# Kernel optimization log

Hardware: AMD Instinct MI355X
Metric: run time of the kernel (lower is better)

The kernel has to match this reference:

```python
import jax, jax.numpy as jnp
import numpy as np

EPS = 1e-5
NUM_HEAD = 8
HEAD_DIM = 64
SCALE = HEAD_DIM ** -0.5


def setup_inputs() -> dict:
    key = jax.random.key(0)
    ks = jax.random.split(key, 3)
    b, n, dim = 4, 2048, 512
    inner = NUM_HEAD * HEAD_DIM  # 512
    x = jax.random.normal(ks[0], (b, n, dim), dtype=jnp.float32)
    ln_w = jnp.ones((dim,), jnp.float32)
    ln_b = jnp.zeros((dim,), jnp.float32)
    qkv_w = jax.random.normal(ks[1], (3 * inner, dim), jnp.float32) * (dim ** -0.5)
    qkv_b = jnp.zeros((3 * inner,), jnp.float32)
    out_w = jax.random.normal(ks[2], (dim, inner), jnp.float32) * (inner ** -0.5)
    out_b = jnp.zeros((dim,), jnp.float32)
    return {"x": x, "ln_w": ln_w, "ln_b": ln_b, "qkv_w": qkv_w,
            "qkv_b": qkv_b, "out_w": out_w, "out_b": out_b}


def reference(x, ln_w, ln_b, qkv_w, qkv_b, out_w, out_b):
    b, n, dim = x.shape
    # Pre-norm LayerNorm
    mu = jnp.mean(x, axis=-1, keepdims=True)
    var = jnp.mean(jnp.square(x - mu), axis=-1, keepdims=True)
    xn = (x - mu) * jax.lax.rsqrt(var + EPS) * ln_w + ln_b
    # QKV projection (torch Linear: y = x @ W.T + b)
    qkv = xn @ qkv_w.T + qkv_b  # [b, n, 3*inner]
    q, k, v = jnp.split(qkv, 3, axis=-1)
    def heads(t):  # [b, n, inner] -> [b, h, n, d]
        return t.reshape(b, n, NUM_HEAD, HEAD_DIM).transpose(0, 2, 1, 3)
    q, k, v = heads(q), heads(k), heads(v)
    # Naive full attention (materializes [b, h, n, n])
    dots = jnp.einsum('bhqd,bhkd->bhqk', q, k) * SCALE
    attn = jax.nn.softmax(dots, axis=-1)
    o = jnp.einsum('bhqk,bhkd->bhqd', attn, v)
    o = o.transpose(0, 2, 1, 3).reshape(b, n, NUM_HEAD * HEAD_DIM)
    return o @ out_w.T + out_b
```

## Files before the change

kernel.cpp:

```cpp
#include <hip/hip_runtime.h>

typedef __attribute__((ext_vector_type(8))) short bf16x8;
typedef __attribute__((ext_vector_type(4))) float floatx4;

#define B_    4
#define N_    2048
#define DIM_  512
#define NH_   8
#define HD_   64
#define SCALE_ 0.125f
#define SL2E_ (0.125f * 1.44269504f)

__device__ __forceinline__ unsigned short f32_to_bf16(float f) {
    unsigned int u = __float_as_uint(f);
    u += 0x7FFFu + ((u >> 16) & 1u);
    return (unsigned short)(u >> 16);
}

__device__ __forceinline__ float bf16_to_f32(unsigned short u) {
    return __uint_as_float(((unsigned int)u) << 16);
}

__device__ __forceinline__ floatx4 mfma16(bf16x8 a, bf16x8 b, floatx4 c) {
    return __builtin_amdgcn_mfma_f32_16x16x32_bf16(a, b, c, 0, 0, 0);
}

__device__ __forceinline__ floatx4 fzero4() {
    floatx4 z = {0.f, 0.f, 0.f, 0.f};
    return z;
}

__device__ __forceinline__ void async16(const unsigned short* g, unsigned short* l) {
    __builtin_amdgcn_global_load_lds((const __attribute__((address_space(1))) void*)g,
                                     (__attribute__((address_space(3))) void*)l,
                                     16, 0, 0);
}

__global__ __launch_bounds__(256) void ln_kernel(const float* __restrict__ x,
                                                 const float* __restrict__ w,
                                                 const float* __restrict__ b,
                                                 unsigned short* __restrict__ xn) {
    int row = blockIdx.x;
    int tid = threadIdx.x;
    int lane = tid & 63, wid = tid >> 6;
    const float2 v = ((const float2*)(x + (size_t)row * DIM_))[tid];
    float s = v.x + v.y;
    float sq = v.x * v.x + v.y * v.y;
#pragma unroll
    for (int off = 1; off < 64; off <<= 1) {
        s  += __shfl_xor(s, off, 64);
        sq += __shfl_xor(sq, off, 64);
    }
    __shared__ float red[2][4];
    if (lane == 0) { red[0][wid] = s; red[1][wid] = sq; }
    __syncthreads();
    s  = red[0][0] + red[0][1] + red[0][2] + red[0][3];
    sq = red[1][0] + red[1][1] + red[1][2] + red[1][3];
    float mu   = s * (1.f / DIM_);
    float var  = sq * (1.f / DIM_) - mu * mu;
    float rstd = rsqrtf(var + 1e-5f);
    float2 wv = ((const float2*)w)[tid];
    float2 bv = ((const float2*)b)[tid];
    float y0 = (v.x - mu) * rstd * wv.x + bv.x;
    float y1 = (v.y - mu) * rstd * wv.y + bv.y;
    unsigned int pack = (unsigned int)f32_to_bf16(y0) |
                        ((unsigned int)f32_to_bf16(y1) << 16);
    ((unsigned int*)xn)[(size_t)row * (DIM_ / 2) + tid] = pack;
}

__global__ __launch_bounds__(256) void cvt_kernel(const float* __restrict__ srcA, int na,
                                                  const float* __restrict__ srcB, int nb,
                                                  unsigned short* __restrict__ dstA,
                                                  unsigned short* __restrict__ dstB) {
    int idx = blockIdx.x * 256 + threadIdx.x;
    if (idx < na)            dstA[idx] = f32_to_bf16(srcA[idx]);
    else if (idx < na + nb)  dstB[idx - na] = f32_to_bf16(srcB[idx - na]);
}

#define GEMM_CORE512(A_, B_ptr, am0, bn0)                                           \
    __shared__ unsigned short Alds[2][128][32];                                     \
    __shared__ unsigned short Blds[2][128][32];                                     \
    int tid = threadIdx.x, lane = tid & 63, wid = tid >> 6;                         \
    int l15 = lane & 15, quad = lane >> 4;                                          \
    int wmloc = (wid >> 1) * 32, wnloc = (wid & 1) * 64;                            \
    int sr = lane >> 2;                                                             \
    int sc = (lane & 3) * 8;                                                        \
    int srow0 = 16 * wid;                                                           \
    floatx4 acc[2][4];                                                              \
    _Pragma("unroll")                                                               \
    for (int i = 0; i < 2; i++)                                                     \
        _Pragma("unroll")                                                           \
        for (int j = 0; j < 4; j++) acc[i][j] = fzero4();                           \
    int buf = 0;                                                                    \
    async16(A_ + (size_t)(am0 + srow0 + sr) * DIM_ + sc, &Alds[0][srow0][0]);       \
    async16(B_ptr + (size_t)(bn0 + srow0 + sr) * DIM_ + sc, &Blds[0][srow0][0]);    \
    __syncthreads();                                                                \
    for (int t = 0; t < 16; t++) {                                                  \
        if (t < 15) {                                                               \
            int k0 = (t + 1) * 32;                                                  \
            async16(A_ + (size_t)(am0 + srow0 + sr) * DIM_ + k0 + sc,               \
                    &Alds[buf ^ 1][srow0][0]);                                      \
            async16(B_ptr + (size_t)(bn0 + srow0 + sr) * DIM_ + k0 + sc,            \
                    &Blds[buf ^ 1][srow0][0]);                                      \
        }                                                                           \
        bf16x8 av[2], bv[4];                                                        \
        _Pragma("unroll")                                                           \
        for (int i = 0; i < 2; i++)                                                 \
            av[i] = *(const bf16x8*)(&Alds[buf][wmloc + 16 * i + l15][quad * 8]);   \
        _Pragma("unroll")                                                           \
        for (int j = 0; j < 4; j++)                                                 \
            bv[j] = *(const bf16x8*)(&Blds[buf][wnloc + 16 * j + l15][quad * 8]);   \
        _Pragma("unroll")                                                           \
        for (int i = 0; i < 2; i++)                                                 \
            _Pragma("unroll")                                                       \
            for (int j = 0; j < 4; j++)                                             \
                acc[i][j] = mfma16(av[i], bv[j], acc[i][j]);                        \
        __syncthreads();                                                            \
        buf ^= 1;                                                                   \
    }

__global__ __launch_bounds__(512, 4) void qkv_gemm(const unsigned short* __restrict__ A,
                                                   const unsigned short* __restrict__ Bw,
                                                   const float* __restrict__ bias,
                                                   unsigned short* __restrict__ Qh,
                                                   unsigned short* __restrict__ Kh,
                                                   unsigned short* __restrict__ Vt) {
    int am0 = blockIdx.x * 128, bn0 = blockIdx.y * 128;
    GEMM_CORE512(A, Bw, am0, bn0)

    if (bn0 >= 1024) {
        unsigned short* sc_ = &Alds[0][0][0] + wid * (16 * 40);
        int m0 = am0 + wmloc;
        int bidx = m0 >> 11;
        int t0 = m0 & 2047;
#pragma unroll
        for (int j = 0; j < 4; j++) {
            float bias_n = bias[bn0 + wnloc + 16 * j + l15];
#pragma unroll
            for (int i = 0; i < 2; i++)
#pragma unroll
                for (int r = 0; r < 4; r++)
                    sc_[l15 * 40 + 16 * i + quad * 4 + r] =
                        f32_to_bf16(acc[i][j][r] + bias_n);
            int nr = lane >> 2;
            int rem = (bn0 - 1024) + wnloc + 16 * j + nr;
            int head = rem >> 6, d = rem & 63;
            bf16x8 vv = *(const bf16x8*)(sc_ + nr * 40 + (lane & 3) * 8);
            *(bf16x8*)(Vt + ((size_t)(bidx * NH_ + head) * HD_ + d) * N_ +
                       t0 + (lane & 3) * 8) = vv;
        }
    } else {
#pragma unroll
        for (int i = 0; i < 2; i++) {
#pragma unroll
            for (int j = 0; j < 4; j++) {
                int n = bn0 + wnloc + 16 * j + l15;
                float bias_n = bias[n];
                int which = n >> 9;
                int rem = n & 511;
                int head = rem >> 6;
                int d = rem & 63;
#pragma unroll
                for (int r = 0; r < 4; r++) {
                    int m = am0 + wmloc + 16 * i + quad * 4 + r;
                    int b = m >> 11;
                    int t = m & 2047;
                    float val = acc[i][j][r] + bias_n;
                    if (which == 0) {
                        Qh[((size_t)(b * NH_ + head) * N_ + t) * HD_ + d] =
                            f32_to_bf16(val * SL2E_);
                    } else {
                        Kh[((size_t)(b * NH_ + head) * N_ + t) * HD_ + d] =
                            f32_to_bf16(val);
                    }
                }
            }
        }
    }
}

__global__ __launch_bounds__(512, 4) void out_gemm(const unsigned short* __restrict__ A,
                                                   const unsigned short* __restrict__ Bw,
                                                   const float* __restrict__ bias,
                                                   float* __restrict__ out) {
    int am0 = blockIdx.x * 128, bn0 = blockIdx.y * 128;
    GEMM_CORE512(A, Bw, am0, bn0)

#pragma unroll
    for (int i = 0; i < 2; i++) {
#pragma unroll
        for (int j = 0; j < 4; j++) {
            int n = bn0 + wnloc + 16 * j + l15;
            float bias_n = bias[n];
#pragma unroll
            for (int r = 0; r < 4; r++) {
                int m = am0 + wmloc + 16 * i + quad * 4 + r;
                out[(size_t)m * DIM_ + n] = acc[i][j][r] + bias_n;
            }
        }
    }
}

__global__ __launch_bounds__(256, 4) void attn_kernel(const unsigned short* __restrict__ Qh,
                                                      const unsigned short* __restrict__ Kh,
                                                      const unsigned short* __restrict__ Vtg,
                                                      unsigned short* __restrict__ Opart,
                                                      float* __restrict__ lpart) {
    int bh = blockIdx.y;
    int b = bh >> 3, head = bh & 7;
    int qt = blockIdx.x;
    int split = blockIdx.z;
    int kv0 = split << 10;
    int tid = threadIdx.x, lane = tid & 63, w = tid >> 6;
    int l15 = lane & 15, quad = lane >> 4;

    const unsigned short* Qp = Qh + (size_t)bh * N_ * HD_;
    const unsigned short* Kg = Kh + (size_t)bh * N_ * HD_;
    const unsigned short* Vg = Vtg + (size_t)bh * HD_ * N_;

    int q0 = qt * 128 + w * 32;

    bf16x8 aQ[2][2];
#pragma unroll
    for (int mh = 0; mh < 2; mh++) {
        const unsigned short* qrow = Qp + (size_t)(q0 + mh * 16 + l15) * HD_ + quad * 8;
        aQ[mh][0] = *(const bf16x8*)(qrow);
        aQ[mh][1] = *(const bf16x8*)(qrow + 32);
    }

    floatx4 of[2][4];
#pragma unroll
    for (int mh = 0; mh < 2; mh++)
#pragma unroll
        for (int t = 0; t < 4; t++) of[mh][t] = fzero4();
    floatx4 lacc[2];
    lacc[0] = fzero4(); lacc[1] = fzero4();

    const short onebf = (short)0x3F80;
    bf16x8 ones = {onebf, onebf, onebf, onebf, onebf, onebf, onebf, onebf};

    __shared__ unsigned short Kt[64][64];
    __shared__ unsigned short Vs[64][64];
    __shared__ unsigned short Pl[4][32][72];

    int srow = lane >> 3;
    int scol = ((lane & 7) ^ srow) * 8;

    int swz0 = (quad ^ (l15 & 7)) * 8;
    int swz1 = ((quad + 4) ^ (l15 & 7)) * 8;

    unsigned short* myP = &Pl[w][0][0];
    for (int kv = kv0; kv < kv0 + 1024; kv += 64) {
#pragma unroll
        for (int i = 0; i < 2; i++) {
            int r0 = 16 * w + 8 * i;
            async16(Kg + (size_t)(kv + r0 + srow) * HD_ + scol, &Kt[r0][0]);
            async16(Vg + (size_t)(r0 + srow) * N_ + kv + scol, &Vs[r0][0]);
        }
        __syncthreads();
        bf16x8 kf[8];
#pragma unroll
        for (int h = 0; h < 4; h++) {
            kf[2 * h]     = *(const bf16x8*)(&Kt[16 * h + l15][swz0]);
            kf[2 * h + 1] = *(const bf16x8*)(&Kt[16 * h + l15][swz1]);
        }
#pragma unroll
        for (int mh = 0; mh < 2; mh++) {
            floatx4 c[4];
#pragma unroll
            for (int h = 0; h < 4; h++) {
                floatx4 cc = fzero4();
                cc = mfma16(aQ[mh][0], kf[2 * h], cc);
                cc = mfma16(aQ[mh][1], kf[2 * h + 1], cc);
                c[h] = cc;
            }
            unsigned short* pw = myP + (mh * 16 + quad * 4) * 72 + l15;
#pragma unroll
            for (int h = 0; h < 4; h++)
#pragma unroll
                for (int r = 0; r < 4; r++)
                    pw[r * 72 + h * 16] = f32_to_bf16(exp2f(c[h][r]));
        }
        bf16x8 vf[8];
#pragma unroll
        for (int t = 0; t < 4; t++) {
            vf[2 * t]     = *(const bf16x8*)(&Vs[16 * t + l15][swz0]);
            vf[2 * t + 1] = *(const bf16x8*)(&Vs[16 * t + l15][swz1]);
        }
#pragma unroll
        for (int mh = 0; mh < 2; mh++) {
            const unsigned short* pr = myP + (mh * 16 + l15) * 72;
            bf16x8 aP0 = *(const bf16x8*)(pr + quad * 8);
            bf16x8 aP1 = *(const bf16x8*)(pr + 32 + quad * 8);
#pragma unroll
            for (int t = 0; t < 4; t++) {
                of[mh][t] = mfma16(aP0, vf[2 * t], of[mh][t]);
                of[mh][t] = mfma16(aP1, vf[2 * t + 1], of[mh][t]);
            }
            lacc[mh] = mfma16(aP0, ones, lacc[mh]);
            lacc[mh] = mfma16(aP1, ones, lacc[mh]);
        }
        __syncthreads();
    }

    unsigned short* Od = Opart + (size_t)split * B_ * N_ * DIM_;
#pragma unroll
    for (int mh = 0; mh < 2; mh++) {
        float inv[4];
#pragma unroll
        for (int r = 0; r < 4; r++) inv[r] = 1.f / lacc[mh][r];
#pragma unroll
        for (int t = 0; t < 4; t++) {
#pragma unroll
            for (int r = 0; r < 4; r++) {
                int t_tok = q0 + mh * 16 + quad * 4 + r;
                int d = 16 * t + l15;
                Od[((size_t)b * N_ + t_tok) * DIM_ + head * HD_ + d] =
                    f32_to_bf16(of[mh][t][r] * inv[r]);
            }
        }
        if (l15 == 0) {
#pragma unroll
            for (int r = 0; r < 4; r++) {
                int t_tok = q0 + mh * 16 + quad * 4 + r;
                lpart[(size_t)split * B_ * NH_ * N_ + (size_t)bh * N_ + t_tok] =
                    lacc[mh][r];
            }
        }
    }
}

__global__ __launch_bounds__(256) void combine_kernel(const unsigned short* __restrict__ Opart,
                                                      const float* __restrict__ lpart,
                                                      unsigned short* __restrict__ Obuf) {
    int idx = blockIdx.x * 256 + threadIdx.x;
    int row = idx >> 7;
    int head = (idx & 127) >> 4;
    int b = row >> 11, t = row & 2047;
    size_t li = (size_t)(b * NH_ + head) * N_ + t;
    float l1 = lpart[li];
    float l2 = lpart[(size_t)B_ * NH_ * N_ + li];
    float s = 1.f / (l1 + l2);
    float w1 = l1 * s, w2 = l2 * s;
    const size_t half = (size_t)B_ * N_ * DIM_;
    ushort4 a = ((const ushort4*)Opart)[idx];
    ushort4 c = ((const ushort4*)(Opart + half))[idx];
    ushort4 o;
    o.x = f32_to_bf16(w1 * bf16_to_f32(a.x) + w2 * bf16_to_f32(c.x));
    o.y = f32_to_bf16(w1 * bf16_to_f32(a.y) + w2 * bf16_to_f32(c.y));
    o.z = f32_to_bf16(w1 * bf16_to_f32(a.z) + w2 * bf16_to_f32(c.z));
    o.w = f32_to_bf16(w1 * bf16_to_f32(a.w) + w2 * bf16_to_f32(c.w));
    ((ushort4*)Obuf)[idx] = o;
}

extern "C" void kernel_launch(void* const* d_in, const int* in_sizes, int n_in,
                              void* d_out, int out_size, void* d_ws, size_t ws_size,
                              hipStream_t stream) {
    const float* x     = (const float*)d_in[0];
    const float* ln_w  = (const float*)d_in[1];
    const float* ln_b  = (const float*)d_in[2];
    const float* qkv_w = (const float*)d_in[3];
    const float* qkv_b = (const float*)d_in[4];
    const float* out_w = (const float*)d_in[5];
    const float* out_b = (const float*)d_in[6];
    float* out = (float*)d_out;

    char* ws = (char*)d_ws;
    const size_t TOK = (size_t)B_ * N_;
    unsigned short* xn    = (unsigned short*)ws;  ws += TOK * DIM_ * 2;
    unsigned short* wq_bf = (unsigned short*)ws;  ws += (size_t)3 * DIM_ * DIM_ * 2;
    unsigned short* wo_bf = (unsigned short*)ws;  ws += (size_t)DIM_ * DIM_ * 2;
    unsigned short* Qh    = (unsigned short*)ws;  ws += TOK * DIM_ * 2;
    unsigned short* Kh    = (unsigned short*)ws;  ws += TOK * DIM_ * 2;
    unsigned short* Vt    = (unsigned short*)ws;  ws += TOK * DIM_ * 2;
    unsigned short* Obuf  = (unsigned short*)ws;  ws += TOK * DIM_ * 2;
    unsigned short* Opart = (unsigned short*)ws;  ws += (size_t)2 * TOK * DIM_ * 2;
    float*          lpart = (float*)ws;           ws += (size_t)2 * B_ * NH_ * N_ * 4;

    const int NW = 3 * DIM_ * DIM_;
    const int NO = DIM_ * DIM_;

    ln_kernel<<<TOK, 256, 0, stream>>>(x, ln_w, ln_b, xn);
    cvt_kernel<<<(NW + NO + 255) / 256, 256, 0, stream>>>(qkv_w, NW, out_w, NO, wq_bf, wo_bf);
    qkv_gemm<<<dim3(TOK / 128, (3 * DIM_) / 128), 512, 0, stream>>>(xn, wq_bf, qkv_b, Qh, Kh, Vt);
    attn_kernel<<<dim3(N_ / 128, B_ * NH_, 2), 256, 0, stream>>>(Qh, Kh, Vt, Opart, lpart);
    combine_kernel<<<(TOK * DIM_) / 4 / 256, 256, 0, stream>>>(Opart, lpart, Obuf);
    out_gemm<<<dim3(TOK / 128, DIM_ / 128), 512, 0, stream>>>(Obuf, wo_bf, out_b, out);
}
```

Baseline: 182.4 us.

## Fuse split-KV combine into output projection GEMM A-tile staging

Removes the separate combine kernel and its Obuf round-trip. The output GEMM now reads both partial attention outputs and their softmax sums while staging A tiles, merges them in registers and writes bf16 into LDS. The GEMM is retiled to 64x128 blocks of 256 threads with a double-buffered loop. This cuts one launch and the 8 MB write plus read of Obuf, but A staging becomes synchronous global loads with extra ALU work, and the operand reads grow because each B tile is read by more blocks.

```diff
diff --git a/kernel.cpp b/kernel.cpp
--- a/kernel.cpp
+++ b/kernel.cpp
@@ -179,12 +179,93 @@
     }
 }
 
-__global__ __launch_bounds__(512, 4) void out_gemm(const unsigned short* __restrict__ A,
-                                                   const unsigned short* __restrict__ Bw,
-                                                   const float* __restrict__ bias,
-                                                   float* __restrict__ out) {
-    int am0 = blockIdx.x * 128, bn0 = blockIdx.y * 128;
-    GEMM_CORE512(A, Bw, am0, bn0)
+__global__ __launch_bounds__(256, 4) void out_gemm_fused(const unsigned short* __restrict__ Opart,
+                                                         const float* __restrict__ lpart,
+                                                         const unsigned short* __restrict__ Bw,
+                                                         const float* __restrict__ bias,
+                                                         float* __restrict__ out) {
+    __shared__ unsigned short Alds[2][64][36];
+    __shared__ unsigned short Blds[2][128][32];
+    int tid = threadIdx.x, lane = tid & 63, wid = tid >> 6;
+    int l15 = lane & 15, quad = lane >> 4;
+    int wmloc = (wid >> 1) * 32, wnloc = (wid & 1) * 64;
+    int am0 = blockIdx.x * 64, bn0 = blockIdx.y * 128;
+
+    int arow = tid >> 2;
+    int ac8 = (tid & 3) * 8;
+    int token = am0 + arow;
+    int bb = token >> 11;
+    const size_t LSTR = (size_t)B_ * NH_ * N_;
+    const size_t OSTR = (size_t)B_ * N_ * DIM_;
+    const unsigned short* arow0 = Opart + (size_t)token * DIM_;
+    const unsigned short* arow1 = arow0 + OSTR;
+
+    int sr = lane >> 2;
+    int sc = (lane & 3) * 8;
+
+    floatx4 acc[2][4];
+#pragma unroll
+    for (int i = 0; i < 2; i++)
+#pragma unroll
+        for (int j = 0; j < 4; j++) acc[i][j] = fzero4();
+
+#define STAGE_A(BUF, T)                                                         \
+    {                                                                           \
+        int k0 = (T) * 32;                                                      \
+        int head = k0 >> 6;                                                     \
+        size_t li = (size_t)(bb * NH_ + head) * N_ + (token & 2047);            \
+        float l1 = lpart[li];                                                   \
+        float l2 = lpart[LSTR + li];                                            \
+        float inv = 1.f / (l1 + l2);                                            \
+        float w1 = l1 * inv, w2 = l2 * inv;                                     \
+        bf16x8 o0 = *(const bf16x8*)(arow0 + k0 + ac8);                         \
+        bf16x8 o1 = *(const bf16x8*)(arow1 + k0 + ac8);                         \
+        bf16x8 pk;                                                              \
+        _Pragma("unroll")                                                       \
+        for (int e = 0; e < 8; e++)                                             \
+            pk[e] = (short)f32_to_bf16(                                         \
+                w1 * bf16_to_f32((unsigned short)o0[e]) +                       \
+                w2 * bf16_to_f32((unsigned short)o1[e]));                       \
+        *(bf16x8*)(&Alds[BUF][arow][ac8]) = pk;                                 \
+    }
+
+#define STAGE_B(BUF, T)                                                         \
+    {                                                                           \
+        int k0 = (T) * 32;                                                      \
+        _Pragma("unroll")                                                       \
+        for (int i = 0; i < 2; i++) {                                           \
+            int r0 = 32 * wid + 16 * i;                                         \
+            async16(Bw + (size_t)(bn0 + r0 + sr) * DIM_ + k0 + sc,              \
+                    &Blds[BUF][r0][0]);                                         \
+        }                                                                       \
+    }
+
+    STAGE_B(0, 0)
+    STAGE_A(0, 0)
+    __syncthreads();
+    int buf = 0;
+    for (int t = 0; t < 16; t++) {
+        if (t < 15) {
+            STAGE_B(buf ^ 1, t + 1)
+            STAGE_A(buf ^ 1, t + 1)
+        }
+        bf16x8 av[2], bv[4];
+#pragma unroll
+        for (int i = 0; i < 2; i++)
+            av[i] = *(const bf16x8*)(&Alds[buf][wmloc + 16 * i + l15][quad * 8]);
+#pragma unroll
+        for (int j = 0; j < 4; j++)
+            bv[j] = *(const bf16x8*)(&Blds[buf][wnloc + 16 * j + l15][quad * 8]);
+#pragma unroll
+        for (int i = 0; i < 2; i++)
+#pragma unroll
+            for (int j = 0; j < 4; j++)
+                acc[i][j] = mfma16(av[i], bv[j], acc[i][j]);
+        __syncthreads();
+        buf ^= 1;
+    }
+#undef STAGE_A
+#undef STAGE_B
 
 #pragma unroll
     for (int i = 0; i < 2; i++) {
@@ -330,29 +411,6 @@
     }
 }
 
-__global__ __launch_bounds__(256) void combine_kernel(const unsigned short* __restrict__ Opart,
-                                                      const float* __restrict__ lpart,
-                                                      unsigned short* __restrict__ Obuf) {
-    int idx = blockIdx.x * 256 + threadIdx.x;
-    int row = idx >> 7;
-    int head = (idx & 127) >> 4;
-    int b = row >> 11, t = row & 2047;
-    size_t li = (size_t)(b * NH_ + head) * N_ + t;
-    float l1 = lpart[li];
-    float l2 = lpart[(size_t)B_ * NH_ * N_ + li];
-    float s = 1.f / (l1 + l2);
-    float w1 = l1 * s, w2 = l2 * s;
-    const size_t half = (size_t)B_ * N_ * DIM_;
-    ushort4 a = ((const ushort4*)Opart)[idx];
-    ushort4 c = ((const ushort4*)(Opart + half))[idx];
-    ushort4 o;
-    o.x = f32_to_bf16(w1 * bf16_to_f32(a.x) + w2 * bf16_to_f32(c.x));
-    o.y = f32_to_bf16(w1 * bf16_to_f32(a.y) + w2 * bf16_to_f32(c.y));
-    o.z = f32_to_bf16(w1 * bf16_to_f32(a.z) + w2 * bf16_to_f32(c.z));
-    o.w = f32_to_bf16(w1 * bf16_to_f32(a.w) + w2 * bf16_to_f32(c.w));
-    ((ushort4*)Obuf)[idx] = o;
-}
-
 extern "C" void kernel_launch(void* const* d_in, const int* in_sizes, int n_in,
                               void* d_out, int out_size, void* d_ws, size_t ws_size,
                               hipStream_t stream) {
@@ -373,7 +431,6 @@
     unsigned short* Qh    = (unsigned short*)ws;  ws += TOK * DIM_ * 2;
     unsigned short* Kh    = (unsigned short*)ws;  ws += TOK * DIM_ * 2;
     unsigned short* Vt    = (unsigned short*)ws;  ws += TOK * DIM_ * 2;
-    unsigned short* Obuf  = (unsigned short*)ws;  ws += TOK * DIM_ * 2;
     unsigned short* Opart = (unsigned short*)ws;  ws += (size_t)2 * TOK * DIM_ * 2;
     float*          lpart = (float*)ws;           ws += (size_t)2 * B_ * NH_ * N_ * 4;
 
@@ -384,6 +441,5 @@
     cvt_kernel<<<(NW + NO + 255) / 256, 256, 0, stream>>>(qkv_w, NW, out_w, NO, wq_bf, wo_bf);
     qkv_gemm<<<dim3(TOK / 128, (3 * DIM_) / 128), 512, 0, stream>>>(xn, wq_bf, qkv_b, Qh, Kh, Vt);
     attn_kernel<<<dim3(N_ / 128, B_ * NH_, 2), 256, 0, stream>>>(Qh, Kh, Vt, Opart, lpart);
-    combine_kernel<<<(TOK * DIM_) / 4 / 256, 256, 0, stream>>>(Opart, lpart, Obuf);
-    out_gemm<<<dim3(TOK / 128, DIM_ / 128), 512, 0, stream>>>(Obuf, wo_bf, out_b, out);
-}
+    out_gemm_fused<<<dim3(TOK / 64, DIM_ / 128), 256, 0, stream>>>(Opart, lpart, wo_bf, out_b, out);
+}
```

New measurement: 182.3 us. About the same (-0.0%).
